# Kernel optimization log

Hardware: AMD Instinct MI355X
Metric: run time of the kernel (lower is better)

Reference implementation:

```python
import jax, jax.numpy as jnp
import numpy as np

N_NODES = 50000
N_EDGES = 800000
IN_FEAT = 128
N_CLASSES = 64
K_HOPS = 2


def setup_inputs() -> dict:
    key = jax.random.key(0)
    k1, k2, k3, k4 = jax.random.split(key, 4)
    x = jax.random.normal(k1, (N_NODES, IN_FEAT), dtype=jnp.float32)
    edge_index = jax.random.randint(k2, (2, N_EDGES), 0, N_NODES, dtype=jnp.int64)
    # Linear layer params (PyTorch-style Kaiming-uniform-ish scale)
    lim = 1.0 / np.sqrt(IN_FEAT)
    W = jax.random.uniform(k3, (N_CLASSES, IN_FEAT), jnp.float32, -lim, lim)
    b = jax.random.uniform(k4, (N_CLASSES,), jnp.float32, -lim, lim)
    return {"x": x, "edge_index": edge_index, "W": W, "b": b}


def _sg_propagate(x, edge_index, K):
    """K-hop GCN-normalized propagation with self-loops (SGConv)."""
    N = x.shape[0]
    loop = jnp.arange(N, dtype=edge_index.dtype)
    row = jnp.concatenate([edge_index[0], loop])  # source nodes
    col = jnp.concatenate([edge_index[1], loop])  # target nodes
    deg = jax.ops.segment_sum(jnp.ones_like(col, dtype=x.dtype), col, num_segments=N)
    dinv = jnp.where(deg > 0, jax.lax.rsqrt(deg), 0.0)
    norm = dinv[row] * dinv[col]  # [E+N]
    for _ in range(K):
        x = jax.ops.segment_sum(norm[:, None] * x[row], col, num_segments=N)
    return x


def reference(x, edge_index, W, b):
    h = _sg_propagate(x, edge_index, K_HOPS)  # [N, in_features]
    return h @ W.T + b  # [N, num_classes]
```

## Files before the change

kernel.cpp:

```cpp
#include <hip/hip_runtime.h>
#include <hip/hip_fp16.h>

#define N_NODES   50000
#define N_EDGES   800000
#define IN_FEAT   128
#define N_CLASSES 64
#define LDS_PAD   132

__global__ void zero_cnt_kernel(int* __restrict__ cnt, int n) {
    int i = blockIdx.x * blockDim.x + threadIdx.x;
    if (i < n) cnt[i] = 0;
}

__global__ void count_rank_kernel(const int* __restrict__ col, int* __restrict__ cnt,
                                  int* __restrict__ rank, int e) {
    int i = (blockIdx.x * blockDim.x + threadIdx.x) * 4;
    if (i + 3 < e) {
        int4 c = *(const int4*)(col + i);
        int r0 = atomicAdd(&cnt[c.x], 1);
        int r1 = atomicAdd(&cnt[c.y], 1);
        int r2 = atomicAdd(&cnt[c.z], 1);
        int r3 = atomicAdd(&cnt[c.w], 1);
        *(int4*)(rank + i) = make_int4(r0, r1, r2, r3);
    } else {
        for (int k = i; k < e; ++k) rank[k] = atomicAdd(&cnt[col[k]], 1);
    }
}

__global__ __launch_bounds__(256) void block_sum_kernel(const int* __restrict__ cnt,
                                                        int* __restrict__ bsum, int n) {
    __shared__ int s[256];
    int t = threadIdx.x;
    int i = blockIdx.x * 256 + t;
    s[t] = (i < n) ? cnt[i] : 0;
    __syncthreads();
    for (int off = 128; off > 0; off >>= 1) {
        if (t < off) s[t] += s[t + off];
        __syncthreads();
    }
    if (t == 0) bsum[blockIdx.x] = s[0];
}

__global__ __launch_bounds__(256) void apply_scan_kernel(const int* __restrict__ cnt,
                                                         const int* __restrict__ bsum,
                                                         int* __restrict__ rowptr,
                                                         float* __restrict__ dinv,
                                                         int n, int nch) {
    __shared__ int sb[256];
    __shared__ int s[256];
    int b = blockIdx.x, t = threadIdx.x;

    sb[t] = (t < nch) ? bsum[t] : 0;
    __syncthreads();
    for (int off = 1; off < 256; off <<= 1) {
        int add = (t >= off) ? sb[t - off] : 0;
        __syncthreads();
        sb[t] += add;
        __syncthreads();
    }

    int i = b * 256 + t;
    int v = (i < n) ? cnt[i] : 0;
    s[t] = v;
    __syncthreads();
    for (int off = 1; off < 256; off <<= 1) {
        int add = (t >= off) ? s[t - off] : 0;
        __syncthreads();
        s[t] += add;
        __syncthreads();
    }
    int boff = (b > 0) ? sb[b - 1] : 0;
    if (i < n) {
        rowptr[i] = boff + s[t] - v;
        dinv[i]   = rsqrtf((float)(v + 1));
    }
    if (i == n - 1) rowptr[n] = boff + s[t];
}

__global__ void scatter_kernel(const int* __restrict__ row, const int* __restrict__ col,
                               const int* __restrict__ rank, const int* __restrict__ rowptr,
                               unsigned short* __restrict__ adj, int e) {
    int i = (blockIdx.x * blockDim.x + threadIdx.x) * 4;
    if (i + 3 < e) {
        int4 r  = *(const int4*)(row + i);
        int4 c  = *(const int4*)(col + i);
        int4 rk = *(const int4*)(rank + i);
        adj[rowptr[c.x] + rk.x] = (unsigned short)r.x;
        adj[rowptr[c.y] + rk.y] = (unsigned short)r.y;
        adj[rowptr[c.z] + rk.z] = (unsigned short)r.z;
        adj[rowptr[c.w] + rk.w] = (unsigned short)r.w;
    } else {
        for (int k = i; k < e; ++k)
            adj[rowptr[col[k]] + rank[k]] = (unsigned short)row[k];
    }
}

__global__ __launch_bounds__(256) void gemm_kernel(const float* __restrict__ x,
                                                   const float* __restrict__ W,
                                                   const float* __restrict__ dinv,
                                                   __half* __restrict__ u, int n) {
    __shared__ float xs[64][LDS_PAD];
    __shared__ float ws[64][LDS_PAD];
    int t = threadIdx.x;
    int rowbase = blockIdx.x * 64;

    for (int i = t; i < 64 * 32; i += 256) {
        int r  = i >> 5;
        int kk = i & 31;
        *(float4*)(&ws[r][kk * 4]) = *(const float4*)(W + (size_t)r * IN_FEAT + kk * 4);
        int gr = rowbase + r;
        float4 v = make_float4(0.f, 0.f, 0.f, 0.f);
        if (gr < n) v = *(const float4*)(x + (size_t)gr * IN_FEAT + kk * 4);
        *(float4*)(&xs[r][kk * 4]) = v;
    }
    __syncthreads();

    int rg = t >> 4;
    int cg = t & 15;
    float acc[4][4] = {};

    for (int kk = 0; kk < 32; ++kk) {
        float4 a[4], bb[4];
#pragma unroll
        for (int i = 0; i < 4; ++i) a[i]  = *(float4*)(&xs[rg + 16 * i][kk * 4]);
#pragma unroll
        for (int j = 0; j < 4; ++j) bb[j] = *(float4*)(&ws[cg + 16 * j][kk * 4]);
#pragma unroll
        for (int i = 0; i < 4; ++i)
#pragma unroll
            for (int j = 0; j < 4; ++j)
                acc[i][j] += a[i].x * bb[j].x + a[i].y * bb[j].y +
                             a[i].z * bb[j].z + a[i].w * bb[j].w;
    }

#pragma unroll
    for (int i = 0; i < 4; ++i) {
        int gr = rowbase + rg + 16 * i;
        if (gr < n) {
            float d = dinv[gr];
#pragma unroll
            for (int j = 0; j < 4; ++j)
                u[(size_t)gr * N_CLASSES + cg + 16 * j] = __float2half(d * acc[i][j]);
        }
    }
}

__global__ __launch_bounds__(256) void hop_sum_kernel(const int* __restrict__ rowptr,
                                                      const unsigned short* __restrict__ adj,
                                                      const float* __restrict__ dinv,
                                                      const __half* __restrict__ yin,
                                                      __half* __restrict__ yout_h,
                                                      float* __restrict__ yout_f,
                                                      const float* __restrict__ bias,
                                                      int mode, int n) {
    int sub  = threadIdx.x >> 6;
    int lane = threadIdx.x & 63;
    int node = blockIdx.x * 4 + sub;
    if (node >= n) return;

    int s  = rowptr[node];
    int e2 = rowptr[node + 1];

    float acc = __half2float(yin[(size_t)node * N_CLASSES + lane]);
    int k = s;
    for (; k + 7 < e2; k += 8) {
        float v0 = __half2float(yin[(size_t)adj[k + 0] * N_CLASSES + lane]);
        float v1 = __half2float(yin[(size_t)adj[k + 1] * N_CLASSES + lane]);
        float v2 = __half2float(yin[(size_t)adj[k + 2] * N_CLASSES + lane]);
        float v3 = __half2float(yin[(size_t)adj[k + 3] * N_CLASSES + lane]);
        float v4 = __half2float(yin[(size_t)adj[k + 4] * N_CLASSES + lane]);
        float v5 = __half2float(yin[(size_t)adj[k + 5] * N_CLASSES + lane]);
        float v6 = __half2float(yin[(size_t)adj[k + 6] * N_CLASSES + lane]);
        float v7 = __half2float(yin[(size_t)adj[k + 7] * N_CLASSES + lane]);
        acc += ((v0 + v1) + (v2 + v3)) + ((v4 + v5) + (v6 + v7));
    }
    for (; k < e2; ++k)
        acc += __half2float(yin[(size_t)adj[k] * N_CLASSES + lane]);

    float d = dinv[node];
    if (mode == 0) {
        yout_h[(size_t)node * N_CLASSES + lane] = __float2half(d * d * acc);
    } else {
        yout_f[(size_t)node * N_CLASSES + lane] = d * acc + bias[lane];
    }
}

extern "C" void kernel_launch(void* const* d_in, const int* in_sizes, int n_in,
                              void* d_out, int out_size, void* d_ws, size_t ws_size,
                              hipStream_t stream) {
    const float* x     = (const float*)d_in[0];
    const int*   edges = (const int*)d_in[1];
    const float* W     = (const float*)d_in[2];
    const float* b     = (const float*)d_in[3];
    float*       out   = (float*)d_out;

    const int* row = edges;
    const int* col = edges + N_EDGES;

    char* ws = (char*)d_ws;
    int*            cnt    = (int*)(ws + 0);
    int*            rowptr = (int*)(ws + 256 * 1024);
    float*          dinv   = (float*)(ws + 512 * 1024);
    int*            bsum   = (int*)(ws + 768 * 1024);
    unsigned short* adj    = (unsigned short*)(ws + 1024 * 1024);
    int*            rank   = (int*)(ws + 4608 * 1024);
    __half*         u      = (__half*)(ws + 8 * 1024 * 1024);
    __half*         w1     = (__half*)(ws + 16 * 1024 * 1024);

    const int nblk  = (N_NODES + 255) / 256;
    const int eblk4 = (N_EDGES / 4 + 255) / 256;

    zero_cnt_kernel<<<nblk, 256, 0, stream>>>(cnt, N_NODES);
    count_rank_kernel<<<eblk4, 256, 0, stream>>>(col, cnt, rank, N_EDGES);
    block_sum_kernel<<<nblk, 256, 0, stream>>>(cnt, bsum, N_NODES);
    apply_scan_kernel<<<nblk, 256, 0, stream>>>(cnt, bsum, rowptr, dinv, N_NODES, nblk);
    scatter_kernel<<<eblk4, 256, 0, stream>>>(row, col, rank, rowptr, adj, N_EDGES);

    gemm_kernel<<<(N_NODES + 63) / 64, 256, 0, stream>>>(x, W, dinv, u, N_NODES);

    hop_sum_kernel<<<(N_NODES + 3) / 4, 256, 0, stream>>>(rowptr, adj, dinv,
        u, w1, nullptr, nullptr, 0, N_NODES);
    hop_sum_kernel<<<(N_NODES + 3) / 4, 256, 0, stream>>>(rowptr, adj, dinv,
        w1, nullptr, out, b, 1, N_NODES);
}
```

Before: 156.8 us.

## Fuse degree counting with the GEMM in one interleaved launch

The edge-count/rank atomics and the x·Wᵀ GEMM now share one launch: even blocks do counting and odd blocks do GEMM tiles. This lets the compute-bound GEMM overlap the atomic-bound counting and removes a kernel launch. Because the GEMM now runs before dinv exists, the per-source dinv scaling moves into the first hop, which does an extra dinv gather per edge. That adds some memory latency to the gather-heavy first propagation pass.

Result: faster. 134.3 us (-14.4%).

```diff
diff --git a/kernel.cpp b/kernel.cpp
--- a/kernel.cpp
+++ b/kernel.cpp
@@ -12,18 +12,69 @@
     if (i < n) cnt[i] = 0;
 }
 
-__global__ void count_rank_kernel(const int* __restrict__ col, int* __restrict__ cnt,
-                                  int* __restrict__ rank, int e) {
-    int i = (blockIdx.x * blockDim.x + threadIdx.x) * 4;
-    if (i + 3 < e) {
-        int4 c = *(const int4*)(col + i);
-        int r0 = atomicAdd(&cnt[c.x], 1);
-        int r1 = atomicAdd(&cnt[c.y], 1);
-        int r2 = atomicAdd(&cnt[c.z], 1);
-        int r3 = atomicAdd(&cnt[c.w], 1);
-        *(int4*)(rank + i) = make_int4(r0, r1, r2, r3);
-    } else {
-        for (int k = i; k < e; ++k) rank[k] = atomicAdd(&cnt[col[k]], 1);
+__global__ __launch_bounds__(256) void count_gemm_kernel(
+        const int* __restrict__ col, int* __restrict__ cnt, int* __restrict__ rank,
+        const float* __restrict__ x, const float* __restrict__ W,
+        __half* __restrict__ y, int e, int n) {
+    __shared__ float xs[64][LDS_PAD];
+    __shared__ float ws[64][LDS_PAD];
+    int idx = (int)blockIdx.x >> 1;
+
+    if ((blockIdx.x & 1) == 0) {
+        int i = (idx * 256 + threadIdx.x) * 4;
+        if (i + 3 < e) {
+            int4 c = *(const int4*)(col + i);
+            int r0 = atomicAdd(&cnt[c.x], 1);
+            int r1 = atomicAdd(&cnt[c.y], 1);
+            int r2 = atomicAdd(&cnt[c.z], 1);
+            int r3 = atomicAdd(&cnt[c.w], 1);
+            *(int4*)(rank + i) = make_int4(r0, r1, r2, r3);
+        } else {
+            for (int k = i; k < e; ++k) rank[k] = atomicAdd(&cnt[col[k]], 1);
+        }
+        return;
+    }
+
+    int t = threadIdx.x;
+    int rowbase = idx * 64;
+
+    for (int i = t; i < 64 * 32; i += 256) {
+        int r  = i >> 5;
+        int kk = i & 31;
+        *(float4*)(&ws[r][kk * 4]) = *(const float4*)(W + (size_t)r * IN_FEAT + kk * 4);
+        int gr = rowbase + r;
+        float4 v = make_float4(0.f, 0.f, 0.f, 0.f);
+        if (gr < n) v = *(const float4*)(x + (size_t)gr * IN_FEAT + kk * 4);
+        *(float4*)(&xs[r][kk * 4]) = v;
+    }
+    __syncthreads();
+
+    int rg = t >> 4;
+    int cg = t & 15;
+    float acc[4][4] = {};
+
+    for (int kk = 0; kk < 32; ++kk) {
+        float4 a[4], bb[4];
+#pragma unroll
+        for (int i = 0; i < 4; ++i) a[i]  = *(float4*)(&xs[rg + 16 * i][kk * 4]);
+#pragma unroll
+        for (int j = 0; j < 4; ++j) bb[j] = *(float4*)(&ws[cg + 16 * j][kk * 4]);
+#pragma unroll
+        for (int i = 0; i < 4; ++i)
+#pragma unroll
+            for (int j = 0; j < 4; ++j)
+                acc[i][j] += a[i].x * bb[j].x + a[i].y * bb[j].y +
+                             a[i].z * bb[j].z + a[i].w * bb[j].w;
+    }
+
+#pragma unroll
+    for (int i = 0; i < 4; ++i) {
+        int gr = rowbase + rg + 16 * i;
+        if (gr < n) {
+#pragma unroll
+            for (int j = 0; j < 4; ++j)
+                y[(size_t)gr * N_CLASSES + cg + 16 * j] = __float2half(acc[i][j]);
+        }
     }
 }
 
@@ -95,56 +146,6 @@
     }
 }
 
-__global__ __launch_bounds__(256) void gemm_kernel(const float* __restrict__ x,
-                                                   const float* __restrict__ W,
-                                                   const float* __restrict__ dinv,
-                                                   __half* __restrict__ u, int n) {
-    __shared__ float xs[64][LDS_PAD];
-    __shared__ float ws[64][LDS_PAD];
-    int t = threadIdx.x;
-    int rowbase = blockIdx.x * 64;
-
-    for (int i = t; i < 64 * 32; i += 256) {
-        int r  = i >> 5;
-        int kk = i & 31;
-        *(float4*)(&ws[r][kk * 4]) = *(const float4*)(W + (size_t)r * IN_FEAT + kk * 4);
-        int gr = rowbase + r;
-        float4 v = make_float4(0.f, 0.f, 0.f, 0.f);
-        if (gr < n) v = *(const float4*)(x + (size_t)gr * IN_FEAT + kk * 4);
-        *(float4*)(&xs[r][kk * 4]) = v;
-    }
-    __syncthreads();
-
-    int rg = t >> 4;
-    int cg = t & 15;
-    float acc[4][4] = {};
-
-    for (int kk = 0; kk < 32; ++kk) {
-        float4 a[4], bb[4];
-#pragma unroll
-        for (int i = 0; i < 4; ++i) a[i]  = *(float4*)(&xs[rg + 16 * i][kk * 4]);
-#pragma unroll
-        for (int j = 0; j < 4; ++j) bb[j] = *(float4*)(&ws[cg + 16 * j][kk * 4]);
-#pragma unroll
-        for (int i = 0; i < 4; ++i)
-#pragma unroll
-            for (int j = 0; j < 4; ++j)
-                acc[i][j] += a[i].x * bb[j].x + a[i].y * bb[j].y +
-                             a[i].z * bb[j].z + a[i].w * bb[j].w;
-    }
-
-#pragma unroll
-    for (int i = 0; i < 4; ++i) {
-        int gr = rowbase + rg + 16 * i;
-        if (gr < n) {
-            float d = dinv[gr];
-#pragma unroll
-            for (int j = 0; j < 4; ++j)
-                u[(size_t)gr * N_CLASSES + cg + 16 * j] = __float2half(d * acc[i][j]);
-        }
-    }
-}
-
 __global__ __launch_bounds__(256) void hop_sum_kernel(const int* __restrict__ rowptr,
                                                       const unsigned short* __restrict__ adj,
                                                       const float* __restrict__ dinv,
@@ -160,27 +161,45 @@
 
     int s  = rowptr[node];
     int e2 = rowptr[node + 1];
-
-    float acc = __half2float(yin[(size_t)node * N_CLASSES + lane]);
+    float d = dinv[node];
+
+    float acc;
     int k = s;
-    for (; k + 7 < e2; k += 8) {
-        float v0 = __half2float(yin[(size_t)adj[k + 0] * N_CLASSES + lane]);
-        float v1 = __half2float(yin[(size_t)adj[k + 1] * N_CLASSES + lane]);
-        float v2 = __half2float(yin[(size_t)adj[k + 2] * N_CLASSES + lane]);
-        float v3 = __half2float(yin[(size_t)adj[k + 3] * N_CLASSES + lane]);
-        float v4 = __half2float(yin[(size_t)adj[k + 4] * N_CLASSES + lane]);
-        float v5 = __half2float(yin[(size_t)adj[k + 5] * N_CLASSES + lane]);
-        float v6 = __half2float(yin[(size_t)adj[k + 6] * N_CLASSES + lane]);
-        float v7 = __half2float(yin[(size_t)adj[k + 7] * N_CLASSES + lane]);
-        acc += ((v0 + v1) + (v2 + v3)) + ((v4 + v5) + (v6 + v7));
-    }
-    for (; k < e2; ++k)
-        acc += __half2float(yin[(size_t)adj[k] * N_CLASSES + lane]);
-
-    float d = dinv[node];
     if (mode == 0) {
+        acc = d * __half2float(yin[(size_t)node * N_CLASSES + lane]);
+        for (; k + 7 < e2; k += 8) {
+            int r0 = adj[k + 0], r1 = adj[k + 1], r2 = adj[k + 2], r3 = adj[k + 3];
+            int r4 = adj[k + 4], r5 = adj[k + 5], r6 = adj[k + 6], r7 = adj[k + 7];
+            float a0 = dinv[r0] * __half2float(yin[(size_t)r0 * N_CLASSES + lane]);
+            float a1 = dinv[r1] * __half2float(yin[(size_t)r1 * N_CLASSES + lane]);
+            float a2 = dinv[r2] * __half2float(yin[(size_t)r2 * N_CLASSES + lane]);
+            float a3 = dinv[r3] * __half2float(yin[(size_t)r3 * N_CLASSES + lane]);
+            float a4 = dinv[r4] * __half2float(yin[(size_t)r4 * N_CLASSES + lane]);
+            float a5 = dinv[r5] * __half2float(yin[(size_t)r5 * N_CLASSES + lane]);
+            float a6 = dinv[r6] * __half2float(yin[(size_t)r6 * N_CLASSES + lane]);
+            float a7 = dinv[r7] * __half2float(yin[(size_t)r7 * N_CLASSES + lane]);
+            acc += ((a0 + a1) + (a2 + a3)) + ((a4 + a5) + (a6 + a7));
+        }
+        for (; k < e2; ++k) {
+            int r = adj[k];
+            acc += dinv[r] * __half2float(yin[(size_t)r * N_CLASSES + lane]);
+        }
         yout_h[(size_t)node * N_CLASSES + lane] = __float2half(d * d * acc);
     } else {
+        acc = __half2float(yin[(size_t)node * N_CLASSES + lane]);
+        for (; k + 7 < e2; k += 8) {
+            float v0 = __half2float(yin[(size_t)adj[k + 0] * N_CLASSES + lane]);
+            float v1 = __half2float(yin[(size_t)adj[k + 1] * N_CLASSES + lane]);
+            float v2 = __half2float(yin[(size_t)adj[k + 2] * N_CLASSES + lane]);
+            float v3 = __half2float(yin[(size_t)adj[k + 3] * N_CLASSES + lane]);
+            float v4 = __half2float(yin[(size_t)adj[k + 4] * N_CLASSES + lane]);
+            float v5 = __half2float(yin[(size_t)adj[k + 5] * N_CLASSES + lane]);
+            float v6 = __half2float(yin[(size_t)adj[k + 6] * N_CLASSES + lane]);
+            float v7 = __half2float(yin[(size_t)adj[k + 7] * N_CLASSES + lane]);
+            acc += ((v0 + v1) + (v2 + v3)) + ((v4 + v5) + (v6 + v7));
+        }
+        for (; k < e2; ++k)
+            acc += __half2float(yin[(size_t)adj[k] * N_CLASSES + lane]);
         yout_f[(size_t)node * N_CLASSES + lane] = d * acc + bias[lane];
     }
 }
@@ -204,22 +223,22 @@
     int*            bsum   = (int*)(ws + 768 * 1024);
     unsigned short* adj    = (unsigned short*)(ws + 1024 * 1024);
     int*            rank   = (int*)(ws + 4608 * 1024);
-    __half*         u      = (__half*)(ws + 8 * 1024 * 1024);
+    __half*         y      = (__half*)(ws + 8 * 1024 * 1024);
     __half*         w1     = (__half*)(ws + 16 * 1024 * 1024);
 
     const int nblk  = (N_NODES + 255) / 256;
     const int eblk4 = (N_EDGES / 4 + 255) / 256;
+    const int gblk  = (N_NODES + 63) / 64;
 
     zero_cnt_kernel<<<nblk, 256, 0, stream>>>(cnt, N_NODES);
-    count_rank_kernel<<<eblk4, 256, 0, stream>>>(col, cnt, rank, N_EDGES);
+    count_gemm_kernel<<<eblk4 + gblk, 256, 0, stream>>>(col, cnt, rank, x, W, y,
+                                                        N_EDGES, N_NODES);
     block_sum_kernel<<<nblk, 256, 0, stream>>>(cnt, bsum, N_NODES);
     apply_scan_kernel<<<nblk, 256, 0, stream>>>(cnt, bsum, rowptr, dinv, N_NODES, nblk);
     scatter_kernel<<<eblk4, 256, 0, stream>>>(row, col, rank, rowptr, adj, N_EDGES);
 
-    gemm_kernel<<<(N_NODES + 63) / 64, 256, 0, stream>>>(x, W, dinv, u, N_NODES);
-
     hop_sum_kernel<<<(N_NODES + 3) / 4, 256, 0, stream>>>(rowptr, adj, dinv,
-        u, w1, nullptr, nullptr, 0, N_NODES);
+        y, w1, nullptr, nullptr, 0, N_NODES);
     hop_sum_kernel<<<(N_NODES + 3) / 4, 256, 0, stream>>>(rowptr, adj, dinv,
         w1, nullptr, out, b, 1, N_NODES);
 }
```
